# Kernel optimization log

Hardware: AMD Instinct MI355X
Metric: run time of the kernel (lower is better)

The kernel has to match this reference:

```python
import jax, jax.numpy as jnp
import numpy as np

H_IN = 1024
H_OUT = 1024
P = 512
DT_MIN = 0.004
DT_MAX = 0.1
STEP_RESCALE = 1.0
MIN_NEG = 1e-3
EPS_LAM = 1e-6
EPS_DIV = 1e-9
CLIP_MAX = 20.0


def _hippo_lambda_raw(p):
    # Mirrors TorchS5.__init__ HiPPO-LegS-style symmetric init.
    idx = np.arange(p, dtype=np.float64)
    Pv = np.sqrt(1.0 + 2.0 * idx)
    A = np.tril(Pv[:, None] * Pv[None, :]) - np.diag(idx)
    A = -A
    Pr = np.sqrt(idx + 0.5)
    S = A + Pr[:, None] * Pr[None, :]
    S_sym = 0.5 * (S + S.T)
    eig = np.linalg.eigvalsh(S_sym).astype(np.float32)
    lambda_init = -np.clip(np.abs(eig), 1e-3, None)
    raw = -np.log(np.expm1(np.clip(-lambda_init, 1e-6, None)))
    return jnp.asarray(raw, dtype=jnp.float32)


def setup_inputs() -> dict:
    key = jax.random.key(0)
    ku, kt, kb, kc = jax.random.split(key, 4)
    Bsz, L = 16, 1024
    u = jax.random.normal(ku, (Bsz, L, H_IN), dtype=jnp.float32)
    timesteps = jax.random.uniform(kt, (Bsz, L), dtype=jnp.float32)
    Lambda_raw = _hippo_lambda_raw(P)
    log_step_init = 0.5 * (np.log(DT_MIN) + np.log(DT_MAX))
    log_step = jnp.full((P,), log_step_init, dtype=jnp.float32)
    # kaiming_uniform_(a=sqrt(5)) -> U(-1/sqrt(fan_in), 1/sqrt(fan_in))
    Bmat = jax.random.uniform(kb, (P, H_IN), dtype=jnp.float32,
                              minval=-1.0, maxval=1.0) / np.sqrt(H_IN)
    Cmat = jax.random.uniform(kc, (H_OUT, P), dtype=jnp.float32,
                              minval=-1.0, maxval=1.0) / np.sqrt(P)
    Dvec = jnp.zeros((H_IN,), dtype=jnp.float32)  # H_in == H_out path
    return {"u": u, "timesteps": timesteps, "Lambda_raw": Lambda_raw,
            "log_step": log_step, "B": Bmat, "C": Cmat, "D": Dvec}


def reference(u, timesteps, Lambda_raw, log_step, B, C, D):
    # u: [B,L,H_in], timesteps: [B,L]
    Bu = jnp.einsum('ph,blh->blp', B, u)                      # [B,L,P]
    step_vec = STEP_RESCALE * jnp.exp(log_step)               # [P]
    Lam = -(jax.nn.softplus(Lambda_raw) + MIN_NEG)            # [P]
    Delta = jnp.maximum(step_vec[None, None, :] * timesteps[..., None], 0.0)
    A_bar = jnp.exp(jnp.minimum(Lam[None, None, :] * Delta, CLIP_MAX))
    # zoh gamma: (exp(Lam*Delta)-1)/Lam, fallback Delta near Lam=0
    gamma = jnp.where(jnp.abs(Lam)[None, None, :] > EPS_LAM,
                      (A_bar - 1.0) / Lam[None, None, :], Delta)
    b_seq = gamma * Bu
    A_cum = jnp.cumprod(A_bar, axis=1)                        # [B,L,P]
    z = b_seq / (A_cum + EPS_DIV)
    s = jnp.cumsum(z, axis=1)
    x_seq = A_cum * s
    ys = jnp.einsum('hp,blp->blh', C, x_seq) + D * u          # [B,L,H_out]
    return ys
```

## Files before the change

kernel.cpp:

```cpp
#include <hip/hip_runtime.h>
#include <cstdint>
#include <cstddef>

#define H_IN   1024
#define H_OUTD 1024
#define PDIM   512
#define BSZ    16
#define LSEQ   1024
#define BLM    (BSZ * LSEQ)
#define CCH    32
#define CLEN   32

typedef __bf16 bf16_t;
typedef __bf16 bf16x8 __attribute__((ext_vector_type(8)));
typedef float  floatx4 __attribute__((ext_vector_type(4)));

__device__ __forceinline__ unsigned short f2bf(float f) {
    unsigned u = __float_as_uint(f);
    u = u + 0x7fffu + ((u >> 16) & 1u);
    return (unsigned short)(u >> 16);
}
__device__ __forceinline__ float bf2f(unsigned short s) {
    return __uint_as_float((unsigned)s << 16);
}

__device__ __forceinline__ void gl_lds16(const void* g, void* l) {
    __builtin_amdgcn_global_load_lds(
        (const __attribute__((address_space(1))) void*)g,
        (__attribute__((address_space(3))) void*)l, 16, 0, 0);
}

#define NU4 (BLM * H_IN / 4)
#define NB4 (PDIM * H_IN / 4)
#define NC4 (H_OUTD * PDIM / 4)
__global__ void setup_kernel(const float* __restrict__ Lraw,
                             const float* __restrict__ lstep,
                             float* __restrict__ stepv,
                             float* __restrict__ lamv,
                             const float4* __restrict__ Usrc,
                             ushort4* __restrict__ Udst,
                             const float4* __restrict__ Bsrc,
                             ushort4* __restrict__ Bdst,
                             const float4* __restrict__ Csrc,
                             ushort4* __restrict__ Cdst) {
    const int gid = blockIdx.x * 256 + threadIdx.x;
    if (gid < PDIM) {
        stepv[gid] = expf(lstep[gid]);
        float x = Lraw[gid];
        float sp = fmaxf(x, 0.0f) + log1pf(expf(-fabsf(x)));
        lamv[gid] = -(sp + 1e-3f);
    }
    if (gid < NU4) {
        float4 v = Usrc[gid];
        ushort4 o;
        o.x = f2bf(v.x); o.y = f2bf(v.y); o.z = f2bf(v.z); o.w = f2bf(v.w);
        Udst[gid] = o;
    } else {
        const int g2 = gid - NU4;
        if (g2 < NB4) {
            float4 v = Bsrc[g2];
            ushort4 o;
            o.x = f2bf(v.x); o.y = f2bf(v.y); o.z = f2bf(v.z); o.w = f2bf(v.w);
            Bdst[g2] = o;
        } else if (g2 < NB4 + NC4) {
            const int g3 = g2 - NB4;
            float4 v = Csrc[g3];
            ushort4 o;
            o.x = f2bf(v.x); o.y = f2bf(v.y); o.z = f2bf(v.z); o.w = f2bf(v.w);
            Cdst[g3] = o;
        }
    }
}

template<int GXL>
__global__ __launch_bounds__(512, 4)
void gemm1_8w(const bf16_t* __restrict__ A, const bf16_t* __restrict__ Bm,
              unsigned short* __restrict__ Cb, int M, int N, int K) {
    __shared__ bf16_t As[2 * 4096];
    __shared__ bf16_t Bs[2 * 4096];

    const int i     = blockIdx.x;
    const int n_blk = (i >> 3) & ((1 << GXL) - 1);
    const int m_blk = ((i >> (3 + GXL)) << 3) | (i & 7);
    const int m0    = m_blk << 7;
    const int n0    = n_blk << 7;

    const int tid  = threadIdx.x;
    const int lane = tid & 63;
    const int w    = tid >> 6;
    const int wm   = (w & 1) << 6;
    const int wn   = (w >> 1) << 5;
    const int r16  = lane & 15;
    const int q    = lane >> 4;
    const int fsw  = ((q ^ ((r16 + (r16 >> 2)) & 3)) << 3);

    const int srow = lane >> 2;
    const int seg  = (lane & 3) ^ ((srow + (srow >> 2)) & 3);
    const int cw   = w << 4;

    const bf16_t* gA = A  + (size_t)(m0 + cw + srow) * K + seg * 8;
    const bf16_t* gB = Bm + (size_t)(n0 + cw + srow) * K + seg * 8;
    bf16_t* lA = &As[cw * 32];
    bf16_t* lB = &Bs[cw * 32];

    floatx4 acc[4][2] = {};

    gl_lds16(gA, lA);
    gl_lds16(gB, lB);
    __syncthreads();

    int cur = 0;
    for (int k0 = 0; k0 < K; k0 += 32) {
        const int nxt = cur ^ 1;
        if (k0 + 32 < K) {
            gl_lds16(gA + k0 + 32, lA + nxt * 4096);
            gl_lds16(gB + k0 + 32, lB + nxt * 4096);
        }

        const bf16_t* rA = As + cur * 4096;
        const bf16_t* rB = Bs + cur * 4096;
        bf16x8 af[4], bfr[2];
#pragma unroll
        for (int ii = 0; ii < 4; ++ii)
            af[ii]  = *(const bf16x8*)&rA[(wm + ii * 16 + r16) * 32 + fsw];
#pragma unroll
        for (int ii = 0; ii < 2; ++ii)
            bfr[ii] = *(const bf16x8*)&rB[(wn + ii * 16 + r16) * 32 + fsw];
#pragma unroll
        for (int mi = 0; mi < 4; ++mi)
#pragma unroll
            for (int ni = 0; ni < 2; ++ni)
                acc[mi][ni] = __builtin_amdgcn_mfma_f32_16x16x32_bf16(
                    af[mi], bfr[ni], acc[mi][ni], 0, 0, 0);

        __syncthreads();
        cur = nxt;
    }

#pragma unroll
    for (int mi = 0; mi < 4; ++mi) {
#pragma unroll
        for (int e = 0; e < 4; ++e) {
            const int m = m0 + wm + mi * 16 + q * 4 + e;
#pragma unroll
            for (int ni = 0; ni < 2; ++ni) {
                const int n = n0 + wn + ni * 16 + r16;
                Cb[(size_t)m * N + n] = f2bf(acc[mi][ni][e]);
            }
        }
    }
}

template<int GXL>
__global__ __launch_bounds__(256, 4)
void gemm2_nt(const bf16_t* __restrict__ A, const bf16_t* __restrict__ Bm,
              float* __restrict__ Cf, int M, int N, int K,
              const float* __restrict__ Dv, const float* __restrict__ U32) {
    __shared__ bf16_t As[2 * 4096];
    __shared__ bf16_t Bs[2 * 4096];

    const int i     = blockIdx.x;
    const int n_blk = (i >> 3) & ((1 << GXL) - 1);
    const int m_blk = ((i >> (3 + GXL)) << 3) | (i & 7);
    const int m0    = m_blk << 7;
    const int n0    = n_blk << 7;

    const int tid  = threadIdx.x;
    const int lane = tid & 63;
    const int w    = tid >> 6;
    const int wm   = (w & 1) << 6;
    const int wn   = (w >> 1) << 6;
    const int r16  = lane & 15;
    const int q    = lane >> 4;
    const int fsw  = ((q ^ ((r16 + (r16 >> 2)) & 3)) << 3);

    const int srow = lane >> 2;
    const int seg  = (lane & 3) ^ ((srow + (srow >> 2)) & 3);
    const int c0   = w * 32;
    const int c1   = c0 + 16;

    const bf16_t* gA0 = A  + (size_t)(m0 + c0 + srow) * K + seg * 8;
    const bf16_t* gA1 = A  + (size_t)(m0 + c1 + srow) * K + seg * 8;
    const bf16_t* gB0 = Bm + (size_t)(n0 + c0 + srow) * K + seg * 8;
    const bf16_t* gB1 = Bm + (size_t)(n0 + c1 + srow) * K + seg * 8;
    bf16_t* lA0 = &As[c0 * 32];
    bf16_t* lA1 = &As[c1 * 32];
    bf16_t* lB0 = &Bs[c0 * 32];
    bf16_t* lB1 = &Bs[c1 * 32];

    floatx4 acc[4][4] = {};

    gl_lds16(gA0, lA0);
    gl_lds16(gA1, lA1);
    gl_lds16(gB0, lB0);
    gl_lds16(gB1, lB1);
    __syncthreads();

    int cur = 0;
    for (int k0 = 0; k0 < K; k0 += 32) {
        const int nxt = cur ^ 1;
        if (k0 + 32 < K) {
            gl_lds16(gA0 + k0 + 32, lA0 + nxt * 4096);
            gl_lds16(gA1 + k0 + 32, lA1 + nxt * 4096);
            gl_lds16(gB0 + k0 + 32, lB0 + nxt * 4096);
            gl_lds16(gB1 + k0 + 32, lB1 + nxt * 4096);
        }

        const bf16_t* rA = As + cur * 4096;
        const bf16_t* rB = Bs + cur * 4096;
        bf16x8 af[4], bfr[4];
#pragma unroll
        for (int ii = 0; ii < 4; ++ii) {
            af[ii]  = *(const bf16x8*)&rA[(wm + ii * 16 + r16) * 32 + fsw];
            bfr[ii] = *(const bf16x8*)&rB[(wn + ii * 16 + r16) * 32 + fsw];
        }
#pragma unroll
        for (int mi = 0; mi < 4; ++mi)
#pragma unroll
            for (int ni = 0; ni < 4; ++ni)
                acc[mi][ni] = __builtin_amdgcn_mfma_f32_16x16x32_bf16(
                    af[mi], bfr[ni], acc[mi][ni], 0, 0, 0);

        __syncthreads();
        cur = nxt;
    }

    float dn[4];
#pragma unroll
    for (int ni = 0; ni < 4; ++ni) dn[ni] = Dv[n0 + wn + ni * 16 + r16];
#pragma unroll
    for (int mi = 0; mi < 4; ++mi) {
#pragma unroll
        for (int e = 0; e < 4; ++e) {
            const int m = m0 + wm + mi * 16 + q * 4 + e;
#pragma unroll
            for (int ni = 0; ni < 4; ++ni) {
                const int n = n0 + wn + ni * 16 + r16;
                const size_t idx = (size_t)m * N + n;
                float v = acc[mi][ni][e];
                if (dn[ni] != 0.0f) v += dn[ni] * U32[idx];
                Cf[idx] = v;
            }
        }
    }
}

__global__ __launch_bounds__(512)
void scan_part1(const unsigned short* __restrict__ Bu, const float* __restrict__ ts,
                const float* __restrict__ stepv, const float* __restrict__ lamv,
                float* __restrict__ Pagg, float* __restrict__ Sagg) {
    const int c = blockIdx.x;
    const int b = blockIdx.y;
    const int p = threadIdx.x;

    const float lam  = lamv[p];
    const float stp  = stepv[p];
    const float rlam = 1.0f / lam;
    const bool  lam_big = fabsf(lam) > 1e-6f;

    const unsigned short* bu = Bu + ((size_t)b * LSEQ + c * CLEN) * PDIM + p;
    const float* tb = ts + b * LSEQ + c * CLEN;

    float P = 1.0f, S = 0.0f;
#pragma unroll 8
    for (int i = 0; i < CLEN; ++i) {
        float t     = tb[i];
        float delta = fmaxf(stp * t, 0.0f);
        float e     = fminf(lam * delta, 20.0f);
        float abar  = __expf(e);
        float gamma = lam_big ? (abar - 1.0f) * rlam : delta;
        S = fmaf(abar, S, gamma * bf2f(bu[(size_t)i * PDIM]));
        P *= abar;
    }
    const size_t o = ((size_t)b * CCH + c) * PDIM + p;
    Pagg[o] = P;
    Sagg[o] = S;
}

__global__ __launch_bounds__(512)
void scan_part23(const unsigned short* __restrict__ Bu, const float* __restrict__ ts,
                 const float* __restrict__ stepv, const float* __restrict__ lamv,
                 const float* __restrict__ Pagg, const float* __restrict__ Sagg,
                 unsigned short* __restrict__ Xbf) {
    const int c = blockIdx.x;
    const int b = blockIdx.y;
    const int p = threadIdx.x;

    const float lam  = lamv[p];
    const float stp  = stepv[p];
    const float rlam = 1.0f / lam;
    const bool  lam_big = fabsf(lam) > 1e-6f;

    const float* Pb = Pagg + (size_t)b * CCH * PDIM + p;
    const float* Sb = Sagg + (size_t)b * CCH * PDIM + p;
    float x = 0.0f;
    int cc = 0;
    for (; cc + 4 <= c; cc += 4) {
        float p0 = Pb[(size_t)(cc + 0) * PDIM], s0 = Sb[(size_t)(cc + 0) * PDIM];
        float p1 = Pb[(size_t)(cc + 1) * PDIM], s1 = Sb[(size_t)(cc + 1) * PDIM];
        float p2 = Pb[(size_t)(cc + 2) * PDIM], s2 = Sb[(size_t)(cc + 2) * PDIM];
        float p3 = Pb[(size_t)(cc + 3) * PDIM], s3 = Sb[(size_t)(cc + 3) * PDIM];
        float p01 = p0 * p1, s01 = fmaf(s0, p1, s1);
        float p23 = p2 * p3, s23 = fmaf(s2, p3, s3);
        float pq  = p01 * p23, sq = fmaf(s01, p23, s23);
        x = fmaf(pq, x, sq);
    }
    for (; cc < c; ++cc) {
        x = fmaf(Pb[(size_t)cc * PDIM], x, Sb[(size_t)cc * PDIM]);
    }

    const unsigned short* bu = Bu + ((size_t)b * LSEQ + c * CLEN) * PDIM + p;
    const float* tb = ts + b * LSEQ + c * CLEN;
    unsigned short* xo = Xbf + ((size_t)b * LSEQ + c * CLEN) * PDIM + p;

#pragma unroll 8
    for (int i = 0; i < CLEN; ++i) {
        float t     = tb[i];
        float delta = fmaxf(stp * t, 0.0f);
        float e     = fminf(lam * delta, 20.0f);
        float abar  = __expf(e);
        float gamma = lam_big ? (abar - 1.0f) * rlam : delta;
        x = fmaf(abar, x, gamma * bf2f(bu[(size_t)i * PDIM]));
        xo[(size_t)i * PDIM] = f2bf(x);
    }
}

extern "C" void kernel_launch(void* const* d_in, const int* in_sizes, int n_in,
                              void* d_out, int out_size, void* d_ws, size_t ws_size,
                              hipStream_t stream) {
    (void)in_sizes; (void)n_in; (void)out_size; (void)ws_size;
    const float* u  = (const float*)d_in[0];
    const float* ts = (const float*)d_in[1];
    const float* Lr = (const float*)d_in[2];
    const float* ls = (const float*)d_in[3];
    const float* Bm = (const float*)d_in[4];
    const float* Cm = (const float*)d_in[5];
    const float* Dv = (const float*)d_in[6];
    float* out = (float*)d_out;

    char* ws = (char*)d_ws;
    bf16_t*         u_bf = (bf16_t*)(ws);
    bf16_t*         B_bf = (bf16_t*)(ws + (32u << 20));
    bf16_t*         C_bf = (bf16_t*)(ws + (33u << 20));
    unsigned short* Bu   = (unsigned short*)(ws + (34u << 20));
    unsigned short* X_bf = (unsigned short*)(ws + (50u << 20));
    float*          Pagg = (float*)(ws + (66u << 20));
    float*          Sagg = (float*)(ws + (67u << 20));
    float*          stepv= (float*)(ws + (69u << 20));
    float*          lamv = stepv + PDIM;

    setup_kernel<<<(NU4 + NB4 + NC4) / 256, 256, 0, stream>>>(
        Lr, ls, stepv, lamv,
        (const float4*)u,  (ushort4*)u_bf,
        (const float4*)Bm, (ushort4*)B_bf,
        (const float4*)Cm, (ushort4*)C_bf);

    gemm1_8w<2><<<512, 512, 0, stream>>>(
        u_bf, B_bf, Bu, BLM, PDIM, H_IN);

    scan_part1<<<dim3(CCH, BSZ), 512, 0, stream>>>(Bu, ts, stepv, lamv, Pagg, Sagg);
    scan_part23<<<dim3(CCH, BSZ), 512, 0, stream>>>(Bu, ts, stepv, lamv,
                                                    Pagg, Sagg, X_bf);

    gemm2_nt<3><<<1024, 256, 0, stream>>>(
        (const bf16_t*)X_bf, C_bf, out, BLM, H_OUTD, PDIM, Dv, u);
}
```

Before: 186.1 us.

## Fuse fp32-to-bf16 conversion of u into first GEMM's A-tile loading

Stops converting the full u activation tensor to bf16 in a separate pass. The first GEMM now loads fp32 u straight from global memory into registers, packs it to bf16 and writes it into shared memory after the MFMA work, with the double buffering kept. This removes a 64MB read plus 32MB write and shrinks the workspace. In exchange the A operand no longer uses the async global-to-LDS path, which adds register pressure and VALU work inside the GEMM, and since u is reused across the N blocks it now re-reads fp32 data at twice the bytes.

```diff
diff --git a/kernel.cpp b/kernel.cpp
--- a/kernel.cpp
+++ b/kernel.cpp
@@ -23,6 +23,9 @@
 __device__ __forceinline__ float bf2f(unsigned short s) {
     return __uint_as_float((unsigned)s << 16);
 }
+__device__ __forceinline__ unsigned pk2(float lo, float hi) {
+    return (unsigned)f2bf(lo) | ((unsigned)f2bf(hi) << 16);
+}
 
 __device__ __forceinline__ void gl_lds16(const void* g, void* l) {
     __builtin_amdgcn_global_load_lds(
@@ -30,15 +33,12 @@
         (__attribute__((address_space(3))) void*)l, 16, 0, 0);
 }
 
-#define NU4 (BLM * H_IN / 4)
 #define NB4 (PDIM * H_IN / 4)
 #define NC4 (H_OUTD * PDIM / 4)
 __global__ void setup_kernel(const float* __restrict__ Lraw,
                              const float* __restrict__ lstep,
                              float* __restrict__ stepv,
                              float* __restrict__ lamv,
-                             const float4* __restrict__ Usrc,
-                             ushort4* __restrict__ Udst,
                              const float4* __restrict__ Bsrc,
                              ushort4* __restrict__ Bdst,
                              const float4* __restrict__ Csrc,
@@ -50,20 +50,14 @@
         float sp = fmaxf(x, 0.0f) + log1pf(expf(-fabsf(x)));
         lamv[gid] = -(sp + 1e-3f);
     }
-    if (gid < NU4) {
-        float4 v = Usrc[gid];
+    if (gid < NB4) {
+        float4 v = Bsrc[gid];
         ushort4 o;
         o.x = f2bf(v.x); o.y = f2bf(v.y); o.z = f2bf(v.z); o.w = f2bf(v.w);
-        Udst[gid] = o;
+        Bdst[gid] = o;
     } else {
-        const int g2 = gid - NU4;
-        if (g2 < NB4) {
-            float4 v = Bsrc[g2];
-            ushort4 o;
-            o.x = f2bf(v.x); o.y = f2bf(v.y); o.z = f2bf(v.z); o.w = f2bf(v.w);
-            Bdst[g2] = o;
-        } else if (g2 < NB4 + NC4) {
-            const int g3 = g2 - NB4;
+        const int g3 = gid - NB4;
+        if (g3 < NC4) {
             float4 v = Csrc[g3];
             ushort4 o;
             o.x = f2bf(v.x); o.y = f2bf(v.y); o.z = f2bf(v.z); o.w = f2bf(v.w);
@@ -74,8 +68,8 @@
 
 template<int GXL>
 __global__ __launch_bounds__(512, 4)
-void gemm1_8w(const bf16_t* __restrict__ A, const bf16_t* __restrict__ Bm,
-              unsigned short* __restrict__ Cb, int M, int N, int K) {
+void gemm1_8w_a32(const float* __restrict__ A32, const bf16_t* __restrict__ Bm,
+                  unsigned short* __restrict__ Cb, int M, int N, int K) {
     __shared__ bf16_t As[2 * 4096];
     __shared__ bf16_t Bs[2 * 4096];
 
@@ -94,26 +88,40 @@
     const int q    = lane >> 4;
     const int fsw  = ((q ^ ((r16 + (r16 >> 2)) & 3)) << 3);
 
+    const int cw   = w << 4;
+
     const int srow = lane >> 2;
     const int seg  = (lane & 3) ^ ((srow + (srow >> 2)) & 3);
-    const int cw   = w << 4;
-
-    const bf16_t* gA = A  + (size_t)(m0 + cw + srow) * K + seg * 8;
     const bf16_t* gB = Bm + (size_t)(n0 + cw + srow) * K + seg * 8;
-    bf16_t* lA = &As[cw * 32];
     bf16_t* lB = &Bs[cw * 32];
 
+    const int arowL = lane >> 2;
+    const int asl   = lane & 3;
+    const int aseg  = asl ^ ((arowL + (arowL >> 2)) & 3);
+    const float* gA32 = A32 + (size_t)(m0 + cw + arowL) * K + aseg * 8;
+    const int aoff  = (cw + arowL) * 32 + asl * 8;
+
     floatx4 acc[4][2] = {};
-
-    gl_lds16(gA, lA);
+    float4 a0, a1;
+
+    a0 = *(const float4*)(gA32);
+    a1 = *(const float4*)(gA32 + 4);
     gl_lds16(gB, lB);
+    {
+        uint4 wv;
+        wv.x = pk2(a0.x, a0.y); wv.y = pk2(a0.z, a0.w);
+        wv.z = pk2(a1.x, a1.y); wv.w = pk2(a1.z, a1.w);
+        *(uint4*)&As[aoff] = wv;
+    }
     __syncthreads();
 
     int cur = 0;
     for (int k0 = 0; k0 < K; k0 += 32) {
         const int nxt = cur ^ 1;
-        if (k0 + 32 < K) {
-            gl_lds16(gA + k0 + 32, lA + nxt * 4096);
+        const bool pf = (k0 + 32 < K);
+        if (pf) {
+            a0 = *(const float4*)(gA32 + k0 + 32);
+            a1 = *(const float4*)(gA32 + k0 + 36);
             gl_lds16(gB + k0 + 32, lB + nxt * 4096);
         }
 
@@ -133,6 +141,12 @@
                 acc[mi][ni] = __builtin_amdgcn_mfma_f32_16x16x32_bf16(
                     af[mi], bfr[ni], acc[mi][ni], 0, 0, 0);
 
+        if (pf) {
+            uint4 wv;
+            wv.x = pk2(a0.x, a0.y); wv.y = pk2(a0.z, a0.w);
+            wv.z = pk2(a1.x, a1.y); wv.w = pk2(a1.z, a1.w);
+            *(uint4*)&As[nxt * 4096 + aoff] = wv;
+        }
         __syncthreads();
         cur = nxt;
     }
@@ -339,24 +353,22 @@
     float* out = (float*)d_out;
 
     char* ws = (char*)d_ws;
-    bf16_t*         u_bf = (bf16_t*)(ws);
-    bf16_t*         B_bf = (bf16_t*)(ws + (32u << 20));
-    bf16_t*         C_bf = (bf16_t*)(ws + (33u << 20));
-    unsigned short* Bu   = (unsigned short*)(ws + (34u << 20));
-    unsigned short* X_bf = (unsigned short*)(ws + (50u << 20));
-    float*          Pagg = (float*)(ws + (66u << 20));
-    float*          Sagg = (float*)(ws + (67u << 20));
-    float*          stepv= (float*)(ws + (69u << 20));
+    bf16_t*         B_bf = (bf16_t*)(ws);
+    bf16_t*         C_bf = (bf16_t*)(ws + (1u << 20));
+    unsigned short* Bu   = (unsigned short*)(ws + (2u << 20));
+    unsigned short* X_bf = (unsigned short*)(ws + (18u << 20));
+    float*          Pagg = (float*)(ws + (34u << 20));
+    float*          Sagg = (float*)(ws + (35u << 20));
+    float*          stepv= (float*)(ws + (36u << 20));
     float*          lamv = stepv + PDIM;
 
-    setup_kernel<<<(NU4 + NB4 + NC4) / 256, 256, 0, stream>>>(
+    setup_kernel<<<(NB4 + NC4) / 256, 256, 0, stream>>>(
         Lr, ls, stepv, lamv,
-        (const float4*)u,  (ushort4*)u_bf,
         (const float4*)Bm, (ushort4*)B_bf,
         (const float4*)Cm, (ushort4*)C_bf);
 
-    gemm1_8w<2><<<512, 512, 0, stream>>>(
-        u_bf, B_bf, Bu, BLM, PDIM, H_IN);
+    gemm1_8w_a32<2><<<512, 512, 0, stream>>>(
+        u, B_bf, Bu, BLM, PDIM, H_IN);
 
     scan_part1<<<dim3(CCH, BSZ), 512, 0, stream>>>(Bu, ts, stepv, lamv, Pagg, Sagg);
     scan_part23<<<dim3(CCH, BSZ), 512, 0, stream>>>(Bu, ts, stepv, lamv,
```

Result: slower. 199.2 us (+7.0%).
